# Performance work log

Measured on AMD Instinct MI355X. Metric: run time of the kernel, lower is better.

The kernel has to match this reference:

```python
import jax, jax.numpy as jnp
import numpy as np

N = 100000   # nodes
E = 1600000  # edges
D = 128      # input feature dim
H = 128      # hidden dim
C = 10       # output classes
G = 64       # graphs in batch


def setup_inputs() -> dict:
    key = jax.random.key(0)
    ks = jax.random.split(key, 24)
    s = 0.02
    lin = lambda k, i, o: jax.random.normal(k, (i, o), jnp.float32) * s
    inp = {
        'x': jax.random.normal(ks[0], (N, D), jnp.float32),
        'edge_index': jax.random.randint(ks[1], (2, E), 0, N),
        'batch': jnp.sort(jax.random.randint(ks[2], (N,), 0, G)),
        # GIN conv 0: Linear(D,H)-ReLU-Linear(H,H)
        'w1_0': lin(ks[3], D, H), 'b1_0': jnp.zeros((H,), jnp.float32),
        'w2_0': lin(ks[4], H, H), 'b2_0': jnp.zeros((H,), jnp.float32),
        # GIN conv 1
        'w1_1': lin(ks[5], H, H), 'b1_1': jnp.zeros((H,), jnp.float32),
        'w2_1': lin(ks[6], H, H), 'b2_1': jnp.zeros((H,), jnp.float32),
        # GIN conv 2
        'w1_2': lin(ks[7], H, H), 'b1_2': jnp.zeros((H,), jnp.float32),
        'w2_2': lin(ks[8], H, H), 'b2_2': jnp.zeros((H,), jnp.float32),
        # LayerNorms (applied after layers 0 and 1)
        'ln_g0': jnp.ones((H,), jnp.float32), 'ln_b0': jnp.zeros((H,), jnp.float32),
        'ln_g1': jnp.ones((H,), jnp.float32), 'ln_b1': jnp.zeros((H,), jnp.float32),
        # post_mp: Linear(H,H) -> Dropout -> Linear(H,C)
        'pw1': lin(ks[9], H, H), 'pb1': jnp.zeros((H,), jnp.float32),
        'pw2': lin(ks[10], H, C), 'pb2': jnp.zeros((C,), jnp.float32),
    }
    return inp


def _gin_conv(x, src, dst, w1, b1, w2, b2):
    # GINConv with eps=0: MLP(x + sum_{j->i} x_j)
    agg = jax.ops.segment_sum(x[src], dst, num_segments=N)  # [N, d]
    h = x + agg
    h = jax.nn.relu(h @ w1 + b1) @ w2 + b2
    return h


def _layernorm(x, g, b, eps=1e-5):
    mu = jnp.mean(x, axis=-1, keepdims=True)
    var = jnp.var(x, axis=-1, keepdims=True)
    return (x - mu) * jax.lax.rsqrt(var + eps) * g + b


def reference(x, edge_index, batch,
              w1_0, b1_0, w2_0, b2_0,
              w1_1, b1_1, w2_1, b2_1,
              w1_2, b1_2, w2_2, b2_2,
              ln_g0, ln_b0, ln_g1, ln_b1,
              pw1, pb1, pw2, pb2):
    src, dst = edge_index[0], edge_index[1]
    convs = [(w1_0, b1_0, w2_0, b2_0), (w1_1, b1_1, w2_1, b2_1), (w1_2, b1_2, w2_2, b2_2)]
    lns = [(ln_g0, ln_b0), (ln_g1, ln_b1)]
    emb = x
    h = x
    for i in range(3):
        w1, b1, w2, b2 = convs[i]
        h = _gin_conv(h, src, dst, w1, b1, w2, b2)
        emb = h
        h = jax.nn.relu(h)
        # dropout p=0.25: identity in eval mode
        if i != 2:
            g, b = lns[i]
            h = _layernorm(h, g, b)
    # global mean pool over graphs
    sums = jax.ops.segment_sum(h, batch, num_segments=G)          # [G, H]
    cnts = jax.ops.segment_sum(jnp.ones((N,), h.dtype), batch, num_segments=G)
    pooled = sums / jnp.maximum(cnts, 1.0)[:, None]
    # post_mp (dropout identity in eval)
    z = pooled @ pw1 + pb1
    logits = z @ pw2 + pb2
    return emb, jax.nn.log_softmax(logits, axis=1)
```

## Files before the change

kernel.cpp:

```cpp
#include <hip/hip_runtime.h>

typedef __bf16 bf16_t;
typedef __bf16 bf16x8 __attribute__((ext_vector_type(8)));
typedef float floatx4 __attribute__((ext_vector_type(4)));

constexpr int N = 100000;
constexpr int E = 1600000;
constexpr int H = 128;
constexpr int G = 64;
constexpr int C = 10;
constexpr int NBLK = (N + 255) / 256;

constexpr int FPART = 8;
constexpr int FPART_SZ = (N + FPART - 1) / FPART;
constexpr int BCHUNK = 2048;
constexpr int BBLK = (E + BCHUNK - 1) / BCHUNK;
constexpr int BCAP = 204800;

constexpr int SUBP = 125;
constexpr int SUBSZ = 100;
constexpr int SB = FPART * SUBP;
constexpr int SCAP = 2048;
constexpr int SCHUNK = 8192;

__device__ inline float bflo(unsigned u) {
  return __builtin_bit_cast(float, u << 16);
}
__device__ inline float bfhi(unsigned u) {
  return __builtin_bit_cast(float, u & 0xffff0000u);
}
__device__ inline unsigned short f2b(float f) {
  return __builtin_bit_cast(unsigned short, (bf16_t)f);
}
__device__ inline unsigned pack2(float a, float b) {
  return (unsigned)f2b(a) | ((unsigned)f2b(b) << 16);
}

__global__ __launch_bounds__(256) void tobf_kernel(const float* __restrict__ x,
                                                   uint4* __restrict__ xb) {
  const int g = blockIdx.x * 256 + threadIdx.x;
  const float4 a = *(const float4*)(x + (size_t)g * 8);
  const float4 b = *(const float4*)(x + (size_t)g * 8 + 4);
  uint4 o;
  o.x = pack2(a.x, a.y);
  o.y = pack2(a.z, a.w);
  o.z = pack2(b.x, b.y);
  o.w = pack2(b.z, b.w);
  xb[g] = o;
}

__global__ __launch_bounds__(256) void bucket_kernel(
    const int* __restrict__ src, const int* __restrict__ dst,
    unsigned* __restrict__ buckets, int* __restrict__ bcnt) {
  __shared__ int offS[4][FPART];
  __shared__ int waveExcl[4][FPART];
  __shared__ int cntA[FPART];
  __shared__ int blockExcl[FPART];
  __shared__ int baseS[FPART];
  __shared__ unsigned stage[BCHUNK];
  const int tid = threadIdx.x;
  const int wave = tid >> 6;
  const int lane = tid & 63;
  if (tid < 32) ((int*)offS)[tid] = 0;
  __syncthreads();

  const int e0 = blockIdx.x * BCHUNK + tid * 8;
  int d[8], s[8];
  int nv = 0;
  if (e0 + 8 <= E) {
    const int4 da = *(const int4*)(dst + e0);
    const int4 db = *(const int4*)(dst + e0 + 4);
    const int4 sa = *(const int4*)(src + e0);
    const int4 sb = *(const int4*)(src + e0 + 4);
    d[0] = da.x; d[1] = da.y; d[2] = da.z; d[3] = da.w;
    d[4] = db.x; d[5] = db.y; d[6] = db.z; d[7] = db.w;
    s[0] = sa.x; s[1] = sa.y; s[2] = sa.z; s[3] = sa.w;
    s[4] = sb.x; s[5] = sb.y; s[6] = sb.z; s[7] = sb.w;
    nv = 8;
  } else {
    nv = (e0 < E) ? (E - e0) : 0;
    if (nv > 8) nv = 8;
    for (int j = 0; j < nv; ++j) {
      d[j] = dst[e0 + j];
      s[j] = src[e0 + j];
    }
    for (int j = nv; j < 8; ++j) { d[j] = 0; s[j] = 0; }
  }

  const unsigned long long below = (1ull << lane) - 1ull;

  int pj[8];
  int slotW[8];

#pragma unroll
  for (int j = 0; j < 8; ++j) {
    const bool valid = (j < nv);
    const int p = d[j] / FPART_SZ;
    pj[j] = p;
    unsigned long long mown = 0;
#pragma unroll
    for (int q = 0; q < FPART; ++q) {
      const unsigned long long mq = __ballot(valid && (p == q));
      if (p == q) mown = mq;
    }
    const int cnt = (int)__popcll(mown);
    const int rank = (int)__popcll(mown & below);
    const int base = offS[wave][p];
    if (valid && rank == 0) offS[wave][p] = base + cnt;
    slotW[j] = base + rank;
  }
  __syncthreads();

  if (tid < FPART) {
    int running = 0;
#pragma unroll
    for (int w = 0; w < 4; ++w) {
      waveExcl[w][tid] = running;
      running += offS[w][tid];
    }
    cntA[tid] = running;
    baseS[tid] = atomicAdd(&bcnt[tid], running);
  }
  __syncthreads();
  if (tid < FPART) {
    int ex = 0;
    for (int q = 0; q < tid; ++q) ex += cntA[q];
    blockExcl[tid] = ex;
  }
  __syncthreads();

#pragma unroll
  for (int j = 0; j < 8; ++j) {
    if (j < nv) {
      const int p = pj[j];
      stage[blockExcl[p] + waveExcl[wave][p] + slotW[j]] =
          ((unsigned)s[j] << 14) | (unsigned)(d[j] - p * FPART_SZ);
    }
  }
  __syncthreads();

#pragma unroll
  for (int p = 0; p < FPART; ++p) {
    const int c = cntA[p];
    const int gb = p * BCAP + baseS[p];
    const int lb = blockExcl[p];
    for (int i = tid; i < c; i += 256) buckets[gb + i] = stage[lb + i];
  }
}

__global__ __launch_bounds__(256) void deghist_kernel(
    const unsigned* __restrict__ buckets, const int* __restrict__ bcnt,
    int* __restrict__ deg) {
  __shared__ int cntS[FPART_SZ];
  const int part = blockIdx.x & (FPART - 1);
  const int sub = blockIdx.x >> 3;
  for (int i = threadIdx.x; i < FPART_SZ; i += 256) cntS[i] = 0;
  __syncthreads();
  const int cnt = bcnt[part];
  const int per = (cnt + 7) >> 3;
  const int lo = sub * per;
  const int hi = min(lo + per, cnt);
  const unsigned* b = buckets + part * BCAP;
  for (int i = lo + threadIdx.x; i < hi; i += 256)
    atomicAdd(&cntS[b[i] & 0x3FFFu], 1);
  __syncthreads();
  const int dbase = part * FPART_SZ;
  for (int i = threadIdx.x; i < FPART_SZ; i += 256) {
    const int c = cntS[i];
    if (c) atomicAdd(&deg[dbase + i], c);
  }
}

__global__ __launch_bounds__(256) void subbucket_kernel(
    const unsigned* __restrict__ buckets, const int* __restrict__ bcnt,
    unsigned* __restrict__ subbuck, int* __restrict__ sbcnt) {
  __shared__ unsigned stage[SCHUNK];
  __shared__ int cntA[SUBP];
  __shared__ int cntB[SUBP];
  __shared__ int exclS[SUBP];
  __shared__ int gbase[SUBP];
  __shared__ int scanbuf[128];
  const int part = blockIdx.x & (FPART - 1);
  const int blk = blockIdx.x >> 3;
  const int nblk = gridDim.x >> 3;
  const int tid = threadIdx.x;
  const int cnt = bcnt[part];
  const unsigned* b = buckets + part * BCAP;

  for (int c0 = blk * SCHUNK; c0 < cnt; c0 += nblk * SCHUNK) {
    const int m = min(SCHUNK, cnt - c0);
    if (tid < SUBP) {
      cntA[tid] = 0;
      cntB[tid] = 0;
    }
    __syncthreads();
    for (int i = tid; i < m; i += 256) {
      const unsigned ent = b[c0 + i];
      atomicAdd(&cntA[(int)(ent & 0x3FFFu) / SUBSZ], 1);
    }
    __syncthreads();
    if (tid < 128) scanbuf[tid] = (tid < SUBP) ? cntA[tid] : 0;
    __syncthreads();
    for (int off = 1; off < 128; off <<= 1) {
      int v = 0;
      if (tid < 128 && tid >= off) v = scanbuf[tid - off];
      __syncthreads();
      if (tid < 128) scanbuf[tid] += v;
      __syncthreads();
    }
    if (tid < SUBP) {
      exclS[tid] = scanbuf[tid] - cntA[tid];
      gbase[tid] = atomicAdd(&sbcnt[part * SUBP + tid], cntA[tid]);
    }
    __syncthreads();
    for (int i = tid; i < m; i += 256) {
      const unsigned ent = b[c0 + i];
      const int s = (int)(ent & 0x3FFFu) / SUBSZ;
      const int r = atomicAdd(&cntB[s], 1);
      stage[exclS[s] + r] = ent;
    }
    __syncthreads();
    for (int i = tid; i < m; i += 256) {
      const unsigned ent = stage[i];
      const int s = (int)(ent & 0x3FFFu) / SUBSZ;
      subbuck[(size_t)(part * SUBP + s) * SCAP + gbase[s] + (i - exclS[s])] =
          ent;
    }
    __syncthreads();
  }
}

__global__ __launch_bounds__(256) void partial_kernel(
    const int* __restrict__ deg, int* __restrict__ partials) {
  __shared__ int sm[256];
  const int tid = threadIdx.x;
  const int i = blockIdx.x * 256 + tid;
  sm[tid] = (i < N) ? deg[i] : 0;
  __syncthreads();
  for (int off = 128; off > 0; off >>= 1) {
    if (tid < off) sm[tid] += sm[tid + off];
    __syncthreads();
  }
  if (tid == 0) partials[blockIdx.x] = sm[0];
}

__global__ __launch_bounds__(512) void scanp_kernel(
    const int* __restrict__ partials, int* __restrict__ blockbase) {
  __shared__ int p[512];
  const int t = threadIdx.x;
  p[t] = (t < NBLK) ? partials[t] : 0;
  __syncthreads();
  for (int off = 1; off < 512; off <<= 1) {
    int v = 0;
    if (t >= off) v = p[t - off];
    __syncthreads();
    p[t] += v;
    __syncthreads();
  }
  if (t < NBLK) blockbase[t] = (t == 0) ? 0 : p[t - 1];
}

__global__ __launch_bounds__(256) void expand_kernel(
    const int* __restrict__ deg, const int* __restrict__ blockbase,
    int* __restrict__ rowptr) {
  __shared__ int sm[256];
  const int tid = threadIdx.x;
  const int i = blockIdx.x * 256 + tid;
  const int d = (i < N) ? deg[i] : 0;
  sm[tid] = d;
  __syncthreads();
  for (int off = 1; off < 256; off <<= 1) {
    int v = 0;
    if (tid >= off) v = sm[tid - off];
    __syncthreads();
    sm[tid] += v;
    __syncthreads();
  }
  const int excl = sm[tid] - d + blockbase[blockIdx.x];
  if (i < N) rowptr[i] = excl;
  if (i == N - 1) rowptr[N] = excl + d;
}

__global__ __launch_bounds__(256) void fill3_kernel(
    const unsigned* __restrict__ subbuck, const int* __restrict__ sbcnt,
    const int* __restrict__ rowptr, int* __restrict__ csr_src) {
  __shared__ unsigned ld[SCAP];
  __shared__ int stageS[SCAP];
  __shared__ int hist[SUBSZ];
  __shared__ int cntB[SUBSZ];
  __shared__ int exclS[SUBSZ];
  __shared__ int scanbuf[128];
  const int sb = blockIdx.x;
  const int part = sb / SUBP;
  const int subl = sb % SUBP;
  const int n0 = part * FPART_SZ + subl * SUBSZ;
  const int tid = threadIdx.x;
  const int cnt = sbcnt[sb];
  const unsigned* b = subbuck + (size_t)sb * SCAP;
  if (tid < SUBSZ) {
    hist[tid] = 0;
    cntB[tid] = 0;
  }
  __syncthreads();
  for (int i = tid; i < cnt; i += 256) {
    const unsigned ent = b[i];
    ld[i] = ent;
    atomicAdd(&hist[(int)(ent & 0x3FFFu) - subl * SUBSZ], 1);
  }
  __syncthreads();
  if (tid < 128) scanbuf[tid] = (tid < SUBSZ) ? hist[tid] : 0;
  __syncthreads();
  for (int off = 1; off < 128; off <<= 1) {
    int v = 0;
    if (tid < 128 && tid >= off) v = scanbuf[tid - off];
    __syncthreads();
    if (tid < 128) scanbuf[tid] += v;
    __syncthreads();
  }
  if (tid < SUBSZ) exclS[tid] = scanbuf[tid] - hist[tid];
  __syncthreads();
  for (int i = tid; i < cnt; i += 256) {
    const unsigned ent = ld[i];
    const int j = (int)(ent & 0x3FFFu) - subl * SUBSZ;
    const int r = atomicAdd(&cntB[j], 1);
    stageS[exclS[j] + r] = (int)(ent >> 14);
  }
  __syncthreads();
  const int rp0 = rowptr[n0];
  for (int i = tid; i < cnt; i += 256) csr_src[rp0 + i] = stageS[i];
}

__global__ __launch_bounds__(256) void gather_kernel(
    const uint4* __restrict__ h, const int* __restrict__ rowptr,
    const int* __restrict__ csr_src, uint4* __restrict__ pre) {
  const int node = blockIdx.x * 16 + (threadIdx.x >> 4);
  const int l = threadIdx.x & 15;
  const int r0 = rowptr[node];
  const int r1 = rowptr[node + 1];
  const uint4 v = h[(size_t)node * 16 + l];
  float a0 = bflo(v.x), a1 = bfhi(v.x), a2 = bflo(v.y), a3 = bfhi(v.y);
  float a4 = bflo(v.z), a5 = bfhi(v.z), a6 = bflo(v.w), a7 = bfhi(v.w);
  int s = r0;
  for (; s + 3 < r1; s += 4) {
    const int i0 = csr_src[s], i1 = csr_src[s + 1];
    const int i2 = csr_src[s + 2], i3 = csr_src[s + 3];
    const uint4 u0 = h[(size_t)i0 * 16 + l];
    const uint4 u1 = h[(size_t)i1 * 16 + l];
    const uint4 u2 = h[(size_t)i2 * 16 + l];
    const uint4 u3 = h[(size_t)i3 * 16 + l];
    a0 += bflo(u0.x); a1 += bfhi(u0.x); a2 += bflo(u0.y); a3 += bfhi(u0.y);
    a4 += bflo(u0.z); a5 += bfhi(u0.z); a6 += bflo(u0.w); a7 += bfhi(u0.w);
    a0 += bflo(u1.x); a1 += bfhi(u1.x); a2 += bflo(u1.y); a3 += bfhi(u1.y);
    a4 += bflo(u1.z); a5 += bfhi(u1.z); a6 += bflo(u1.w); a7 += bfhi(u1.w);
    a0 += bflo(u2.x); a1 += bfhi(u2.x); a2 += bflo(u2.y); a3 += bfhi(u2.y);
    a4 += bflo(u2.z); a5 += bfhi(u2.z); a6 += bflo(u2.w); a7 += bfhi(u2.w);
    a0 += bflo(u3.x); a1 += bfhi(u3.x); a2 += bflo(u3.y); a3 += bfhi(u3.y);
    a4 += bflo(u3.z); a5 += bfhi(u3.z); a6 += bflo(u3.w); a7 += bfhi(u3.w);
  }
  for (; s < r1; ++s) {
    const uint4 u = h[(size_t)csr_src[s] * 16 + l];
    a0 += bflo(u.x); a1 += bfhi(u.x); a2 += bflo(u.y); a3 += bfhi(u.y);
    a4 += bflo(u.z); a5 += bfhi(u.z); a6 += bflo(u.w); a7 += bfhi(u.w);
  }
  uint4 o;
  o.x = pack2(a0, a1);
  o.y = pack2(a2, a3);
  o.z = pack2(a4, a5);
  o.w = pack2(a6, a7);
  pre[(size_t)node * 16 + l] = o;
}

template <int MODE>
__global__ __launch_bounds__(256) void mlp_kernel(
    const unsigned short* __restrict__ pre_g,
    const float* __restrict__ w1, const float* __restrict__ b1,
    const float* __restrict__ w2, const float* __restrict__ b2,
    const float* __restrict__ lng, const float* __restrict__ lnb,
    unsigned short* __restrict__ h_out,
    float* __restrict__ emb) {
  __shared__ unsigned short preS[32 * 136];
  __shared__ unsigned short hidS[32 * 136];
  __shared__ float muS[32];
  __shared__ float rsS[32];

  const int tid = threadIdx.x;
  const int wave = tid >> 6;
  const int lane = tid & 63;
  const int quad = lane >> 4;
  const int l16 = lane & 15;

  union F8 { bf16x8 v; bf16_t e[8]; };

  bf16x8 w1f[4][2], w2f[4][2];
#pragma unroll
  for (int nn = 0; nn < 2; ++nn) {
    const int col = wave * 32 + nn * 16 + l16;
#pragma unroll
    for (int kt = 0; kt < 4; ++kt) {
      F8 t1, t2;
#pragma unroll
      for (int j = 0; j < 8; ++j) {
        const int k = kt * 32 + quad * 8 + j;
        t1.e[j] = (bf16_t)w1[k * H + col];
        t2.e[j] = (bf16_t)w2[k * H + col];
      }
      w1f[kt][nn] = t1.v;
      w2f[kt][nn] = t2.v;
    }
  }
  const float b1v[2] = {b1[wave * 32 + l16], b1[wave * 32 + 16 + l16]};
  const float b2v[2] = {b2[wave * 32 + l16], b2[wave * 32 + 16 + l16]};
  float lng0 = 0.f, lng1 = 0.f, lnb0 = 0.f, lnb1 = 0.f;
  const int c2 = (tid * 2) & 127;
  if (MODE == 0) {
    lng0 = lng[c2]; lng1 = lng[c2 + 1];
    lnb0 = lnb[c2]; lnb1 = lnb[c2 + 1];
  }

  for (int tile = blockIdx.x; tile < N / 32; tile += gridDim.x) {
    const size_t base = (size_t)tile * 32 * H;
    {
      const uint4* srcp = (const uint4*)(pre_g + base);
#pragma unroll
      for (int it = 0; it < 2; ++it) {
        const int chunk = it * 256 + tid;
        const int row = chunk >> 4;
        const int colc = (chunk & 15) * 8;
        *(uint4*)&preS[row * 136 + colc] = srcp[chunk];
      }
    }
    __syncthreads();

    {
      floatx4 acc[2][2];
#pragma unroll
      for (int i = 0; i < 2; ++i)
#pragma unroll
        for (int j = 0; j < 2; ++j) acc[i][j] = {0.f, 0.f, 0.f, 0.f};
#pragma unroll
      for (int kt = 0; kt < 4; ++kt) {
        const int kc = kt * 32 + quad * 8;
        const bf16x8 a0 =
            __builtin_bit_cast(bf16x8, *(const uint4*)&preS[l16 * 136 + kc]);
        const bf16x8 a1 = __builtin_bit_cast(
            bf16x8, *(const uint4*)&preS[(16 + l16) * 136 + kc]);
        acc[0][0] = __builtin_amdgcn_mfma_f32_16x16x32_bf16(a0, w1f[kt][0],
                                                            acc[0][0], 0, 0, 0);
        acc[0][1] = __builtin_amdgcn_mfma_f32_16x16x32_bf16(a0, w1f[kt][1],
                                                            acc[0][1], 0, 0, 0);
        acc[1][0] = __builtin_amdgcn_mfma_f32_16x16x32_bf16(a1, w1f[kt][0],
                                                            acc[1][0], 0, 0, 0);
        acc[1][1] = __builtin_amdgcn_mfma_f32_16x16x32_bf16(a1, w1f[kt][1],
                                                            acc[1][1], 0, 0, 0);
      }
#pragma unroll
      for (int mt = 0; mt < 2; ++mt)
#pragma unroll
        for (int nn = 0; nn < 2; ++nn) {
          const int col = wave * 32 + nn * 16 + l16;
#pragma unroll
          for (int r = 0; r < 4; ++r) {
            const int row = mt * 16 + quad * 4 + r;
            const float v = fmaxf(acc[mt][nn][r] + b1v[nn], 0.f);
            hidS[row * 136 + col] = f2b(v);
          }
        }
    }
    __syncthreads();

    {
      floatx4 acc[2][2];
#pragma unroll
      for (int i = 0; i < 2; ++i)
#pragma unroll
        for (int j = 0; j < 2; ++j) acc[i][j] = {0.f, 0.f, 0.f, 0.f};
#pragma unroll
      for (int kt = 0; kt < 4; ++kt) {
        const int kc = kt * 32 + quad * 8;
        const bf16x8 a0 =
            __builtin_bit_cast(bf16x8, *(const uint4*)&hidS[l16 * 136 + kc]);
        const bf16x8 a1 = __builtin_bit_cast(
            bf16x8, *(const uint4*)&hidS[(16 + l16) * 136 + kc]);
        acc[0][0] = __builtin_amdgcn_mfma_f32_16x16x32_bf16(a0, w2f[kt][0],
                                                            acc[0][0], 0, 0, 0);
        acc[0][1] = __builtin_amdgcn_mfma_f32_16x16x32_bf16(a0, w2f[kt][1],
                                                            acc[0][1], 0, 0, 0);
        acc[1][0] = __builtin_amdgcn_mfma_f32_16x16x32_bf16(a1, w2f[kt][0],
                                                            acc[1][0], 0, 0, 0);
        acc[1][1] = __builtin_amdgcn_mfma_f32_16x16x32_bf16(a1, w2f[kt][1],
                                                            acc[1][1], 0, 0, 0);
      }
#pragma unroll
      for (int mt = 0; mt < 2; ++mt)
#pragma unroll
        for (int nn = 0; nn < 2; ++nn) {
          const int col = wave * 32 + nn * 16 + l16;
#pragma unroll
          for (int r = 0; r < 4; ++r) {
            const int row = mt * 16 + quad * 4 + r;
            float v = acc[mt][nn][r] + b2v[nn];
            if (MODE == 0) v = fmaxf(v, 0.f);
            preS[row * 136 + col] = f2b(v);
          }
        }
    }
    __syncthreads();

    if (MODE == 0) {
      const int n = tid >> 3;
      const int j = tid & 7;
      float s = 0.f, sq = 0.f;
#pragma unroll
      for (int t = 0; t < 16; ++t) {
        const float v =
            __builtin_bit_cast(float, (unsigned)preS[n * 136 + j + 8 * t] << 16);
        s += v;
        sq += v * v;
      }
      s += __shfl_xor(s, 1); sq += __shfl_xor(sq, 1);
      s += __shfl_xor(s, 2); sq += __shfl_xor(sq, 2);
      s += __shfl_xor(s, 4); sq += __shfl_xor(sq, 4);
      if (j == 0) {
        const float mu = s * (1.f / H);
        const float var = sq * (1.f / H) - mu * mu;
        muS[n] = mu;
        rsS[n] = rsqrtf(var + 1e-5f);
      }
      __syncthreads();
      unsigned* ho = (unsigned*)(h_out + base);
#pragma unroll
      for (int it = 0; it < 8; ++it) {
        const int idx = it * 512 + tid * 2;
        const int row = idx >> 7;
        const int k = idx & 127;
        const unsigned pr = *(const unsigned*)&preS[row * 136 + k];
        const float mu = muS[row], rs = rsS[row];
        const float v0 = (bflo(pr) - mu) * rs * lng0 + lnb0;
        const float v1 = (bfhi(pr) - mu) * rs * lng1 + lnb1;
        ho[idx >> 1] = pack2(v0, v1);
      }
    } else {
      unsigned* ho = (unsigned*)(h_out + base);
#pragma unroll
      for (int it = 0; it < 8; ++it) {
        const int idx = it * 512 + tid * 2;
        const int row = idx >> 7;
        const int k = idx & 127;
        const unsigned pr = *(const unsigned*)&preS[row * 136 + k];
        const float v0 = bflo(pr);
        const float v1 = bfhi(pr);
        *(float2*)&emb[base + idx] = make_float2(v0, v1);
        ho[idx >> 1] = pack2(fmaxf(v0, 0.f), fmaxf(v1, 0.f));
      }
    }
    __syncthreads();
  }
}

__global__ __launch_bounds__(256) void pool_kernel(
    const uint4* __restrict__ hv, const int* __restrict__ batch,
    float* __restrict__ pooled, float* __restrict__ cnt) {
  __shared__ int bs[256];
  __shared__ float smr[512];
  __shared__ int endS;
  const int tid = threadIdx.x;
  const int c0 = blockIdx.x * 256;
  const int len = min(256, N - c0);
  if (tid < len) bs[tid] = batch[c0 + tid];
  __syncthreads();

  const int nl = tid >> 4;
  const int fg = tid & 15;
  const int wave = tid >> 6;
  const int lane = tid & 63;

  int start = 0;
  while (start < len) {
    const int g = bs[start];
    if (tid == 0) endS = len;
    __syncthreads();
    for (int i = start + tid; i < len; i += 256)
      if (bs[i] != g) atomicMin(&endS, i);
    __syncthreads();
    const int end = endS;

    float a0 = 0.f, a1 = 0.f, a2 = 0.f, a3 = 0.f;
    float a4 = 0.f, a5 = 0.f, a6 = 0.f, a7 = 0.f;
    for (int i = start + nl; i < end; i += 16) {
      const uint4 u = hv[(size_t)(c0 + i) * 16 + fg];
      a0 += bflo(u.x); a1 += bfhi(u.x); a2 += bflo(u.y); a3 += bfhi(u.y);
      a4 += bflo(u.z); a5 += bfhi(u.z); a6 += bflo(u.w); a7 += bfhi(u.w);
    }
    a0 += __shfl_xor(a0, 16); a1 += __shfl_xor(a1, 16);
    a2 += __shfl_xor(a2, 16); a3 += __shfl_xor(a3, 16);
    a4 += __shfl_xor(a4, 16); a5 += __shfl_xor(a5, 16);
    a6 += __shfl_xor(a6, 16); a7 += __shfl_xor(a7, 16);
    a0 += __shfl_xor(a0, 32); a1 += __shfl_xor(a1, 32);
    a2 += __shfl_xor(a2, 32); a3 += __shfl_xor(a3, 32);
    a4 += __shfl_xor(a4, 32); a5 += __shfl_xor(a5, 32);
    a6 += __shfl_xor(a6, 32); a7 += __shfl_xor(a7, 32);
    if (lane < 16) {
      float* d = &smr[wave * 128 + lane * 8];
      d[0] = a0; d[1] = a1; d[2] = a2; d[3] = a3;
      d[4] = a4; d[5] = a5; d[6] = a6; d[7] = a7;
    }
    __syncthreads();
    if (tid < 128) {
      const float s =
          smr[tid] + smr[128 + tid] + smr[256 + tid] + smr[384 + tid];
      atomicAdd(&pooled[g * H + tid], s);
    }
    if (tid == 0) atomicAdd(&cnt[g], (float)(end - start));
    __syncthreads();
    start = end;
  }
}

__global__ __launch_bounds__(128) void head_kernel(
    const float* __restrict__ pooled, const float* __restrict__ cnt,
    const float* __restrict__ pw1, const float* __restrict__ pb1,
    const float* __restrict__ pw2, const float* __restrict__ pb2,
    float* __restrict__ out_logp) {
  __shared__ float p[H];
  __shared__ float z[H];
  __shared__ float l[C];
  const int g = blockIdx.x;
  const int f = threadIdx.x;
  const float c = fmaxf(cnt[g], 1.f);
  p[f] = pooled[g * H + f] / c;
  __syncthreads();
  float a = pb1[f];
  for (int k = 0; k < H; ++k) a += p[k] * pw1[k * H + f];
  z[f] = a;
  __syncthreads();
  if (f < C) {
    float a2 = pb2[f];
    for (int k = 0; k < H; ++k) a2 += z[k] * pw2[k * C + f];
    l[f] = a2;
  }
  __syncthreads();
  if (f == 0) {
    float m = l[0];
    for (int i = 1; i < C; ++i) m = fmaxf(m, l[i]);
    float s = 0.f;
    for (int i = 0; i < C; ++i) s += expf(l[i] - m);
    const float lse = m + logf(s);
    for (int i = 0; i < C; ++i) out_logp[g * C + i] = l[i] - lse;
  }
}

extern "C" void kernel_launch(void* const* d_in, const int* in_sizes, int n_in,
                              void* d_out, int out_size, void* d_ws,
                              size_t ws_size, hipStream_t stream) {
  const float* x = (const float*)d_in[0];
  const int* ei = (const int*)d_in[1];
  const int* src = ei;
  const int* dst = ei + E;
  const int* batch = (const int*)d_in[2];
  const float* w1_0 = (const float*)d_in[3];
  const float* b1_0 = (const float*)d_in[4];
  const float* w2_0 = (const float*)d_in[5];
  const float* b2_0 = (const float*)d_in[6];
  const float* w1_1 = (const float*)d_in[7];
  const float* b1_1 = (const float*)d_in[8];
  const float* w2_1 = (const float*)d_in[9];
  const float* b2_1 = (const float*)d_in[10];
  const float* w1_2 = (const float*)d_in[11];
  const float* b1_2 = (const float*)d_in[12];
  const float* w2_2 = (const float*)d_in[13];
  const float* b2_2 = (const float*)d_in[14];
  const float* ln_g0 = (const float*)d_in[15];
  const float* ln_b0 = (const float*)d_in[16];
  const float* ln_g1 = (const float*)d_in[17];
  const float* ln_b1 = (const float*)d_in[18];
  const float* pw1 = (const float*)d_in[19];
  const float* pb1 = (const float*)d_in[20];
  const float* pw2 = (const float*)d_in[21];
  const float* pb2 = (const float*)d_in[22];

  unsigned short* xb = (unsigned short*)d_ws;
  unsigned short* hb = xb + (size_t)N * H;
  unsigned short* pre = hb + (size_t)N * H;
  float* pooled = (float*)(pre + (size_t)N * H);
  float* cnt = pooled + (size_t)G * H;
  int* deg = (int*)(cnt + G);
  int* rowptr = deg + N;
  int* cursor = rowptr + N + 1;
  int* csr_src = cursor + N;
  int* partials = csr_src + E;
  int* blockbase = partials + NBLK;
  int* bcnt = blockbase + NBLK;
  int* sbcnt = bcnt + FPART;
  unsigned* buckets = (unsigned*)pre;
  unsigned* subbuck = buckets + (size_t)FPART * BCAP;
  float* emb = (float*)d_out;
  float* logp = emb + (size_t)N * H;

  tobf_kernel<<<N * H / (256 * 8), 256, 0, stream>>>(x, (uint4*)xb);

  hipMemsetAsync(deg, 0, (size_t)N * sizeof(int), stream);
  hipMemsetAsync(bcnt, 0, (size_t)(FPART + SB) * sizeof(int), stream);
  bucket_kernel<<<BBLK, 256, 0, stream>>>(src, dst, buckets, bcnt);
  deghist_kernel<<<64, 256, 0, stream>>>(buckets, bcnt, deg);
  subbucket_kernel<<<256, 256, 0, stream>>>(buckets, bcnt, subbuck, sbcnt);
  partial_kernel<<<NBLK, 256, 0, stream>>>(deg, partials);
  scanp_kernel<<<1, 512, 0, stream>>>(partials, blockbase);
  expand_kernel<<<NBLK, 256, 0, stream>>>(deg, blockbase, rowptr);
  fill3_kernel<<<SB, 256, 0, stream>>>(subbuck, sbcnt, rowptr, csr_src);

  gather_kernel<<<N / 16, 256, 0, stream>>>((const uint4*)xb, rowptr, csr_src,
                                            (uint4*)pre);
  mlp_kernel<0><<<2048, 256, 0, stream>>>(pre, w1_0, b1_0, w2_0, b2_0, ln_g0,
                                          ln_b0, hb, nullptr);
  gather_kernel<<<N / 16, 256, 0, stream>>>((const uint4*)hb, rowptr, csr_src,
                                            (uint4*)pre);
  mlp_kernel<0><<<2048, 256, 0, stream>>>(pre, w1_1, b1_1, w2_1, b2_1, ln_g1,
                                          ln_b1, hb, nullptr);
  gather_kernel<<<N / 16, 256, 0, stream>>>((const uint4*)hb, rowptr, csr_src,
                                            (uint4*)pre);
  mlp_kernel<1><<<2048, 256, 0, stream>>>(pre, w1_2, b1_2, w2_2, b2_2, nullptr,
                                          nullptr, hb, emb);

  hipMemsetAsync(pooled, 0, (size_t)(G * H + G) * sizeof(float), stream);
  pool_kernel<<<NBLK, 256, 0, stream>>>((const uint4*)hb, batch, pooled, cnt);
  head_kernel<<<G, 128, 0, stream>>>(pooled, cnt, pw1, pb1, pw2, pb2, logp);
}
```

Measured before the change: 510.2 us.

## Fuse neighbor gather into MLP kernel with ping-pong feature buffers

Folds the CSR neighbor-sum gather into the per-layer MLP kernel, so each block aggregates its 32 nodes straight into shared memory before the MFMA matmuls. This drops the intermediate pre-activation buffer's global write and read and one launch per layer. Because a layer now reads and writes features in the same launch, it alternates between the xb and hb buffers. The grid grows to one block per tile (N/32 blocks), so the per-block weight-fragment setup is repeated for every tile instead of being amortised over several.

```diff
diff --git a/kernel.cpp b/kernel.cpp
--- a/kernel.cpp
+++ b/kernel.cpp
@@ -330,49 +330,10 @@
   for (int i = tid; i < cnt; i += 256) csr_src[rp0 + i] = stageS[i];
 }
 
-__global__ __launch_bounds__(256) void gather_kernel(
-    const uint4* __restrict__ h, const int* __restrict__ rowptr,
-    const int* __restrict__ csr_src, uint4* __restrict__ pre) {
-  const int node = blockIdx.x * 16 + (threadIdx.x >> 4);
-  const int l = threadIdx.x & 15;
-  const int r0 = rowptr[node];
-  const int r1 = rowptr[node + 1];
-  const uint4 v = h[(size_t)node * 16 + l];
-  float a0 = bflo(v.x), a1 = bfhi(v.x), a2 = bflo(v.y), a3 = bfhi(v.y);
-  float a4 = bflo(v.z), a5 = bfhi(v.z), a6 = bflo(v.w), a7 = bfhi(v.w);
-  int s = r0;
-  for (; s + 3 < r1; s += 4) {
-    const int i0 = csr_src[s], i1 = csr_src[s + 1];
-    const int i2 = csr_src[s + 2], i3 = csr_src[s + 3];
-    const uint4 u0 = h[(size_t)i0 * 16 + l];
-    const uint4 u1 = h[(size_t)i1 * 16 + l];
-    const uint4 u2 = h[(size_t)i2 * 16 + l];
-    const uint4 u3 = h[(size_t)i3 * 16 + l];
-    a0 += bflo(u0.x); a1 += bfhi(u0.x); a2 += bflo(u0.y); a3 += bfhi(u0.y);
-    a4 += bflo(u0.z); a5 += bfhi(u0.z); a6 += bflo(u0.w); a7 += bfhi(u0.w);
-    a0 += bflo(u1.x); a1 += bfhi(u1.x); a2 += bflo(u1.y); a3 += bfhi(u1.y);
-    a4 += bflo(u1.z); a5 += bfhi(u1.z); a6 += bflo(u1.w); a7 += bfhi(u1.w);
-    a0 += bflo(u2.x); a1 += bfhi(u2.x); a2 += bflo(u2.y); a3 += bfhi(u2.y);
-    a4 += bflo(u2.z); a5 += bfhi(u2.z); a6 += bflo(u2.w); a7 += bfhi(u2.w);
-    a0 += bflo(u3.x); a1 += bfhi(u3.x); a2 += bflo(u3.y); a3 += bfhi(u3.y);
-    a4 += bflo(u3.z); a5 += bfhi(u3.z); a6 += bflo(u3.w); a7 += bfhi(u3.w);
-  }
-  for (; s < r1; ++s) {
-    const uint4 u = h[(size_t)csr_src[s] * 16 + l];
-    a0 += bflo(u.x); a1 += bfhi(u.x); a2 += bflo(u.y); a3 += bfhi(u.y);
-    a4 += bflo(u.z); a5 += bfhi(u.z); a6 += bflo(u.w); a7 += bfhi(u.w);
-  }
-  uint4 o;
-  o.x = pack2(a0, a1);
-  o.y = pack2(a2, a3);
-  o.z = pack2(a4, a5);
-  o.w = pack2(a6, a7);
-  pre[(size_t)node * 16 + l] = o;
-}
-
 template <int MODE>
-__global__ __launch_bounds__(256) void mlp_kernel(
-    const unsigned short* __restrict__ pre_g,
+__global__ __launch_bounds__(256) void gmlp_kernel(
+    const unsigned short* __restrict__ h_in,
+    const int* __restrict__ rowptr, const int* __restrict__ csr_src,
     const float* __restrict__ w1, const float* __restrict__ b1,
     const float* __restrict__ w2, const float* __restrict__ b2,
     const float* __restrict__ lng, const float* __restrict__ lnb,
@@ -417,17 +378,49 @@
     lnb0 = lnb[c2]; lnb1 = lnb[c2 + 1];
   }
 
+  const uint4* hv = (const uint4*)h_in;
+
   for (int tile = blockIdx.x; tile < N / 32; tile += gridDim.x) {
     const size_t base = (size_t)tile * 32 * H;
-    {
-      const uint4* srcp = (const uint4*)(pre_g + base);
-#pragma unroll
-      for (int it = 0; it < 2; ++it) {
-        const int chunk = it * 256 + tid;
-        const int row = chunk >> 4;
-        const int colc = (chunk & 15) * 8;
-        *(uint4*)&preS[row * 136 + colc] = srcp[chunk];
-      }
+
+#pragma unroll
+    for (int g = 0; g < 2; ++g) {
+      const int row = g * 16 + (tid >> 4);
+      const int node = tile * 32 + row;
+      const int l = tid & 15;
+      const int r0 = rowptr[node];
+      const int r1 = rowptr[node + 1];
+      const uint4 v = hv[(size_t)node * 16 + l];
+      float a0 = bflo(v.x), a1 = bfhi(v.x), a2 = bflo(v.y), a3 = bfhi(v.y);
+      float a4 = bflo(v.z), a5 = bfhi(v.z), a6 = bflo(v.w), a7 = bfhi(v.w);
+      int s = r0;
+      for (; s + 3 < r1; s += 4) {
+        const int i0 = csr_src[s], i1 = csr_src[s + 1];
+        const int i2 = csr_src[s + 2], i3 = csr_src[s + 3];
+        const uint4 u0 = hv[(size_t)i0 * 16 + l];
+        const uint4 u1 = hv[(size_t)i1 * 16 + l];
+        const uint4 u2 = hv[(size_t)i2 * 16 + l];
+        const uint4 u3 = hv[(size_t)i3 * 16 + l];
+        a0 += bflo(u0.x); a1 += bfhi(u0.x); a2 += bflo(u0.y); a3 += bfhi(u0.y);
+        a4 += bflo(u0.z); a5 += bfhi(u0.z); a6 += bflo(u0.w); a7 += bfhi(u0.w);
+        a0 += bflo(u1.x); a1 += bfhi(u1.x); a2 += bflo(u1.y); a3 += bfhi(u1.y);
+        a4 += bflo(u1.z); a5 += bfhi(u1.z); a6 += bflo(u1.w); a7 += bfhi(u1.w);
+        a0 += bflo(u2.x); a1 += bfhi(u2.x); a2 += bflo(u2.y); a3 += bfhi(u2.y);
+        a4 += bflo(u2.z); a5 += bfhi(u2.z); a6 += bflo(u2.w); a7 += bfhi(u2.w);
+        a0 += bflo(u3.x); a1 += bfhi(u3.x); a2 += bflo(u3.y); a3 += bfhi(u3.y);
+        a4 += bflo(u3.z); a5 += bfhi(u3.z); a6 += bflo(u3.w); a7 += bfhi(u3.w);
+      }
+      for (; s < r1; ++s) {
+        const uint4 u = hv[(size_t)csr_src[s] * 16 + l];
+        a0 += bflo(u.x); a1 += bfhi(u.x); a2 += bflo(u.y); a3 += bfhi(u.y);
+        a4 += bflo(u.z); a5 += bfhi(u.z); a6 += bflo(u.w); a7 += bfhi(u.w);
+      }
+      uint4 o;
+      o.x = pack2(a0, a1);
+      o.y = pack2(a2, a3);
+      o.z = pack2(a4, a5);
+      o.w = pack2(a6, a7);
+      *(uint4*)&preS[row * 136 + l * 8] = o;
     }
     __syncthreads();
 
@@ -708,18 +701,15 @@
   expand_kernel<<<NBLK, 256, 0, stream>>>(deg, blockbase, rowptr);
   fill3_kernel<<<SB, 256, 0, stream>>>(subbuck, sbcnt, rowptr, csr_src);
 
-  gather_kernel<<<N / 16, 256, 0, stream>>>((const uint4*)xb, rowptr, csr_src,
-                                            (uint4*)pre);
-  mlp_kernel<0><<<2048, 256, 0, stream>>>(pre, w1_0, b1_0, w2_0, b2_0, ln_g0,
-                                          ln_b0, hb, nullptr);
-  gather_kernel<<<N / 16, 256, 0, stream>>>((const uint4*)hb, rowptr, csr_src,
-                                            (uint4*)pre);
-  mlp_kernel<0><<<2048, 256, 0, stream>>>(pre, w1_1, b1_1, w2_1, b2_1, ln_g1,
-                                          ln_b1, hb, nullptr);
-  gather_kernel<<<N / 16, 256, 0, stream>>>((const uint4*)hb, rowptr, csr_src,
-                                            (uint4*)pre);
-  mlp_kernel<1><<<2048, 256, 0, stream>>>(pre, w1_2, b1_2, w2_2, b2_2, nullptr,
-                                          nullptr, hb, emb);
+  gmlp_kernel<0><<<N / 32, 256, 0, stream>>>(xb, rowptr, csr_src, w1_0, b1_0,
+                                             w2_0, b2_0, ln_g0, ln_b0, hb,
+                                             nullptr);
+  gmlp_kernel<0><<<N / 32, 256, 0, stream>>>(hb, rowptr, csr_src, w1_1, b1_1,
+                                             w2_1, b2_1, ln_g1, ln_b1, xb,
+                                             nullptr);
+  gmlp_kernel<1><<<N / 32, 256, 0, stream>>>(xb, rowptr, csr_src, w1_2, b1_2,
+                                             w2_2, b2_2, nullptr, nullptr, hb,
+                                             emb);
 
   hipMemsetAsync(pooled, 0, (size_t)(G * H + G) * sizeof(float), stream);
   pool_kernel<<<NBLK, 256, 0, stream>>>((const uint4*)hb, batch, pooled, cnt);
```

After: 569.5 us. 1.12x slower.

## Derive CSR row pointers from sub-bucket counts, dropping degree histogram and scans

Applied to the files above, without the earlier changes.

Removes the global degree histogram, the partial-sum, block-scan and expand kernels, and the deg memset. A single-block scan over the 1000 sub-bucket counts now gives each sub-bucket its base offset, and fill3 writes the row pointers itself from its local histogram exclusive scan. This cuts four kernel launches and several passes over N-sized arrays and the bucket buffer from CSR construction. It relies on sub-buckets being contiguous in node order, which holds because partitions and sub-ranges are ordered by node id.

```diff
diff --git a/kernel.cpp b/kernel.cpp
--- a/kernel.cpp
+++ b/kernel.cpp
@@ -148,29 +148,6 @@
   }
 }
 
-__global__ __launch_bounds__(256) void deghist_kernel(
-    const unsigned* __restrict__ buckets, const int* __restrict__ bcnt,
-    int* __restrict__ deg) {
-  __shared__ int cntS[FPART_SZ];
-  const int part = blockIdx.x & (FPART - 1);
-  const int sub = blockIdx.x >> 3;
-  for (int i = threadIdx.x; i < FPART_SZ; i += 256) cntS[i] = 0;
-  __syncthreads();
-  const int cnt = bcnt[part];
-  const int per = (cnt + 7) >> 3;
-  const int lo = sub * per;
-  const int hi = min(lo + per, cnt);
-  const unsigned* b = buckets + part * BCAP;
-  for (int i = lo + threadIdx.x; i < hi; i += 256)
-    atomicAdd(&cntS[b[i] & 0x3FFFu], 1);
-  __syncthreads();
-  const int dbase = part * FPART_SZ;
-  for (int i = threadIdx.x; i < FPART_SZ; i += 256) {
-    const int c = cntS[i];
-    if (c) atomicAdd(&deg[dbase + i], c);
-  }
-}
-
 __global__ __launch_bounds__(256) void subbucket_kernel(
     const unsigned* __restrict__ buckets, const int* __restrict__ bcnt,
     unsigned* __restrict__ subbuck, int* __restrict__ sbcnt) {
@@ -230,60 +207,26 @@
   }
 }
 
-__global__ __launch_bounds__(256) void partial_kernel(
-    const int* __restrict__ deg, int* __restrict__ partials) {
-  __shared__ int sm[256];
-  const int tid = threadIdx.x;
-  const int i = blockIdx.x * 256 + tid;
-  sm[tid] = (i < N) ? deg[i] : 0;
-  __syncthreads();
-  for (int off = 128; off > 0; off >>= 1) {
-    if (tid < off) sm[tid] += sm[tid + off];
-    __syncthreads();
-  }
-  if (tid == 0) partials[blockIdx.x] = sm[0];
-}
-
-__global__ __launch_bounds__(512) void scanp_kernel(
-    const int* __restrict__ partials, int* __restrict__ blockbase) {
-  __shared__ int p[512];
+__global__ __launch_bounds__(1024) void sbscan_kernel(
+    const int* __restrict__ sbcnt, int* __restrict__ sbbase) {
+  __shared__ int p[1024];
   const int t = threadIdx.x;
-  p[t] = (t < NBLK) ? partials[t] : 0;
-  __syncthreads();
-  for (int off = 1; off < 512; off <<= 1) {
+  p[t] = (t < SB) ? sbcnt[t] : 0;
+  __syncthreads();
+  for (int off = 1; off < 1024; off <<= 1) {
     int v = 0;
     if (t >= off) v = p[t - off];
     __syncthreads();
     p[t] += v;
     __syncthreads();
   }
-  if (t < NBLK) blockbase[t] = (t == 0) ? 0 : p[t - 1];
-}
-
-__global__ __launch_bounds__(256) void expand_kernel(
-    const int* __restrict__ deg, const int* __restrict__ blockbase,
-    int* __restrict__ rowptr) {
-  __shared__ int sm[256];
-  const int tid = threadIdx.x;
-  const int i = blockIdx.x * 256 + tid;
-  const int d = (i < N) ? deg[i] : 0;
-  sm[tid] = d;
-  __syncthreads();
-  for (int off = 1; off < 256; off <<= 1) {
-    int v = 0;
-    if (tid >= off) v = sm[tid - off];
-    __syncthreads();
-    sm[tid] += v;
-    __syncthreads();
-  }
-  const int excl = sm[tid] - d + blockbase[blockIdx.x];
-  if (i < N) rowptr[i] = excl;
-  if (i == N - 1) rowptr[N] = excl + d;
+  if (t < SB) sbbase[t] = p[t] - sbcnt[t];
 }
 
 __global__ __launch_bounds__(256) void fill3_kernel(
     const unsigned* __restrict__ subbuck, const int* __restrict__ sbcnt,
-    const int* __restrict__ rowptr, int* __restrict__ csr_src) {
+    const int* __restrict__ sbbase, int* __restrict__ rowptr,
+    int* __restrict__ csr_src) {
   __shared__ unsigned ld[SCAP];
   __shared__ int stageS[SCAP];
   __shared__ int hist[SUBSZ];
@@ -296,6 +239,7 @@
   const int n0 = part * FPART_SZ + subl * SUBSZ;
   const int tid = threadIdx.x;
   const int cnt = sbcnt[sb];
+  const int base = sbbase[sb];
   const unsigned* b = subbuck + (size_t)sb * SCAP;
   if (tid < SUBSZ) {
     hist[tid] = 0;
@@ -317,7 +261,12 @@
     if (tid < 128) scanbuf[tid] += v;
     __syncthreads();
   }
-  if (tid < SUBSZ) exclS[tid] = scanbuf[tid] - hist[tid];
+  if (tid < SUBSZ) {
+    const int ex = scanbuf[tid] - hist[tid];
+    exclS[tid] = ex;
+    rowptr[n0 + tid] = base + ex;
+  }
+  if (sb == SB - 1 && tid == 0) rowptr[N] = base + cnt;
   __syncthreads();
   for (int i = tid; i < cnt; i += 256) {
     const unsigned ent = ld[i];
@@ -326,8 +275,7 @@
     stageS[exclS[j] + r] = (int)(ent >> 14);
   }
   __syncthreads();
-  const int rp0 = rowptr[n0];
-  for (int i = tid; i < cnt; i += 256) csr_src[rp0 + i] = stageS[i];
+  for (int i = tid; i < cnt; i += 256) csr_src[base + i] = stageS[i];
 }
 
 __global__ __launch_bounds__(256) void gather_kernel(
@@ -683,14 +631,11 @@
   unsigned short* pre = hb + (size_t)N * H;
   float* pooled = (float*)(pre + (size_t)N * H);
   float* cnt = pooled + (size_t)G * H;
-  int* deg = (int*)(cnt + G);
-  int* rowptr = deg + N;
-  int* cursor = rowptr + N + 1;
-  int* csr_src = cursor + N;
-  int* partials = csr_src + E;
-  int* blockbase = partials + NBLK;
-  int* bcnt = blockbase + NBLK;
+  int* rowptr = (int*)(cnt + G);
+  int* csr_src = rowptr + N + 1;
+  int* bcnt = csr_src + E;
   int* sbcnt = bcnt + FPART;
+  int* sbbase = sbcnt + SB;
   unsigned* buckets = (unsigned*)pre;
   unsigned* subbuck = buckets + (size_t)FPART * BCAP;
   float* emb = (float*)d_out;
@@ -698,15 +643,12 @@
 
   tobf_kernel<<<N * H / (256 * 8), 256, 0, stream>>>(x, (uint4*)xb);
 
-  hipMemsetAsync(deg, 0, (size_t)N * sizeof(int), stream);
   hipMemsetAsync(bcnt, 0, (size_t)(FPART + SB) * sizeof(int), stream);
   bucket_kernel<<<BBLK, 256, 0, stream>>>(src, dst, buckets, bcnt);
-  deghist_kernel<<<64, 256, 0, stream>>>(buckets, bcnt, deg);
   subbucket_kernel<<<256, 256, 0, stream>>>(buckets, bcnt, subbuck, sbcnt);
-  partial_kernel<<<NBLK, 256, 0, stream>>>(deg, partials);
-  scanp_kernel<<<1, 512, 0, stream>>>(partials, blockbase);
-  expand_kernel<<<NBLK, 256, 0, stream>>>(deg, blockbase, rowptr);
-  fill3_kernel<<<SB, 256, 0, stream>>>(subbuck, sbcnt, rowptr, csr_src);
+  sbscan_kernel<<<1, 1024, 0, stream>>>(sbcnt, sbbase);
+  fill3_kernel<<<SB, 256, 0, stream>>>(subbuck, sbcnt, sbbase, rowptr,
+                                       csr_src);
 
   gather_kernel<<<N / 16, 256, 0, stream>>>((const uint4*)xb, rowptr, csr_src,
                                             (uint4*)pre);
```

Measured after the change: 477.9 us. 6.3% less time.
